# Kernel optimization log

Measured on AMD Instinct MI355X. Metric: run time of the kernel, lower is better.

The kernel has to match this reference:

```python
import jax, jax.numpy as jnp
import numpy as np

TOP_K = 5
EPS = 1e-12  # F.normalize eps

def _l2_normalize(v):
    n = jnp.linalg.norm(v, axis=-1, keepdims=True)
    return v / jnp.maximum(n, EPS)

def setup_inputs() -> dict:
    key = jax.random.key(0)
    k1, k2 = jax.random.split(key)
    B, S, C, M = 4, 2048, 512, 32768
    x = jax.random.normal(k1, (B, S, C), dtype=jnp.float32)
    # xavier_uniform-ish init for the memory table
    bound = np.sqrt(6.0 / (M + C)).astype(np.float32)
    memory_mean = jax.random.uniform(k2, (M, C), dtype=jnp.float32, minval=-bound, maxval=bound)
    return {"x": x, "memory_mean": memory_mean}

def reference(x, memory_mean):
    B, S, C = x.shape
    Mmat = memory_mean  # deterministic=True -> _sample_M returns memory_mean
    q = x.reshape(-1, C)                      # [BS, C]
    qn = _l2_normalize(q)
    mn = _l2_normalize(Mmat)                  # [M, C]
    sim = qn @ mn.T                           # [BS, M] cosine similarity
    scores, idx = jax.lax.top_k(sim, TOP_K)   # [BS, K]
    w = jax.nn.softmax(scores, axis=-1)       # [BS, K]
    gathered = Mmat[idx]                      # [BS, K, C]
    retrieved = jnp.einsum('bk,bkc->bc', w, gathered).reshape(B, S, C)
    out = x + 0.5 * retrieved
    return out
```

## Files before the change

kernel.cpp:

```cpp
#include <hip/hip_runtime.h>
#include <math.h>

using f32x4 = __attribute__((ext_vector_type(4))) float;
typedef __attribute__((ext_vector_type(4))) int i32x4;
typedef __attribute__((ext_vector_type(8))) int i32x8;
typedef unsigned char u8;

#define BS    8192
#define CDIM  512
#define MROWS 32768
#define NC    8
#define CHUNK (MROWS / NC)
#define TN    32
#define TQ    128
#define KTOP  5
#define ITERS (CHUNK / TN)
#define ROWB  512
#define KEY_INIT 0x3FFF8000u
#define SCL   0x7F7F7F7F

__device__ __forceinline__ unsigned enc_key(float s, int n) {
    unsigned u = __float_as_uint(s);
    u ^= (unsigned)((int)u >> 31) | 0x80000000u;
    return (u & 0xFFFF8000u) | (unsigned)n;
}
__device__ __forceinline__ float dec_score(unsigned k) {
    unsigned u = k & 0xFFFF8000u;
    u = (u & 0x80000000u) ? (u ^ 0x80000000u) : ~u;
    return __uint_as_float(u);
}

__device__ __forceinline__ void ins_nb(unsigned (&ks)[KTOP], unsigned k) {
    unsigned t = k;
#pragma unroll
    for (int j = 0; j < KTOP; ++j) {
        unsigned hi = t > ks[j] ? t : ks[j];
        unsigned lo = t > ks[j] ? ks[j] : t;
        ks[j] = hi; t = lo;
    }
}

__device__ __forceinline__ float dpp_fmax16(float x) {
    int t;
    t = __builtin_amdgcn_update_dpp(0, __float_as_int(x), 0xB1, 0xF, 0xF, true);
    x = fmaxf(x, __int_as_float(t));
    t = __builtin_amdgcn_update_dpp(0, __float_as_int(x), 0x4E, 0xF, 0xF, true);
    x = fmaxf(x, __int_as_float(t));
    t = __builtin_amdgcn_update_dpp(0, __float_as_int(x), 0x141, 0xF, 0xF, true);
    x = fmaxf(x, __int_as_float(t));
    t = __builtin_amdgcn_update_dpp(0, __float_as_int(x), 0x140, 0xF, 0xF, true);
    x = fmaxf(x, __int_as_float(t));
    return x;
}

__global__ void nrm_cast2(const float* __restrict__ memM, u8* __restrict__ mn,
                          const float* __restrict__ x, u8* __restrict__ qn) {
    int wave = threadIdx.x >> 6, lane = threadIdx.x & 63;
    int row = blockIdx.x * 4 + wave;
    const float* in;
    u8* out;
    if (row < MROWS) { in = memM + (size_t)row * CDIM; out = mn + (size_t)row * ROWB; }
    else             { int r = row - MROWS; in = x + (size_t)r * CDIM; out = qn + (size_t)r * ROWB; }
    const float* rp = in + lane * 8;
    float4 v0 = *(const float4*)rp;
    float4 v1 = *(const float4*)(rp + 4);
    float ss = v0.x * v0.x + v0.y * v0.y + v0.z * v0.z + v0.w * v0.w
             + v1.x * v1.x + v1.y * v1.y + v1.z * v1.z + v1.w * v1.w;
#pragma unroll
    for (int d = 1; d < 64; d <<= 1) ss += __shfl_xor(ss, d);
    float sc = 1.0f / fmaxf(sqrtf(ss), 1e-12f);
    int lo = __builtin_amdgcn_cvt_pk_fp8_f32(v0.x * sc, v0.y * sc, 0, false);
    lo     = __builtin_amdgcn_cvt_pk_fp8_f32(v0.z * sc, v0.w * sc, lo, true);
    int hi = __builtin_amdgcn_cvt_pk_fp8_f32(v1.x * sc, v1.y * sc, 0, false);
    hi     = __builtin_amdgcn_cvt_pk_fp8_f32(v1.z * sc, v1.w * sc, hi, true);
    uint2 o; o.x = (unsigned)lo; o.y = (unsigned)hi;
    *(uint2*)(out + lane * 8) = o;
}

__device__ __forceinline__ void stage_tile(const u8* __restrict__ mn, int nb,
                                           u8* buf, int wave, int lane) {
    const int r0 = wave * 8;
    const int li = lane & 31, half = lane >> 5;
#pragma unroll
    for (int j = 0; j < 4; ++j) {
        const int row = r0 + 2 * j + half;
        const u8* src = mn + (size_t)(nb + row) * ROWB + ((li ^ (row & 7)) * 16);
        __builtin_amdgcn_global_load_lds(
            (const __attribute__((address_space(1))) void*)src,
            (__attribute__((address_space(3))) void*)(buf + (r0 + 2 * j) * ROWB),
            16, 0, 0);
    }
}

__global__ __launch_bounds__(256, 2) void simtopk(
        const u8* __restrict__ qn, const u8* __restrict__ mn,
        unsigned* __restrict__ cand) {
    __shared__ __align__(16) u8 Bt[2][TN * ROWB];

    const int tid  = threadIdx.x;
    const int wave = tid >> 6, lane = tid & 63;
    const int quad = lane >> 4, c16 = lane & 15;
    const int nc = blockIdx.x;
    const int qt = blockIdx.y;
    const int qw = qt * TQ + wave * 32;
    const int nb0 = nc * CHUNK;

    i32x8 a[2][4];
#pragma unroll
    for (int s = 0; s < 2; ++s) {
        const u8* p = qn + (size_t)(qw + s * 16 + c16) * ROWB + quad * 32;
#pragma unroll
        for (int t = 0; t < 4; ++t) {
            i32x4 lo = *(const i32x4*)(p + t * 128);
            i32x4 hi = *(const i32x4*)(p + t * 128 + 16);
            a[s][t] = __builtin_shufflevector(lo, hi, 0, 1, 2, 3, 4, 5, 6, 7);
        }
    }

    unsigned keys[8][KTOP];
    float thr[8];
#pragma unroll
    for (int l = 0; l < 8; ++l) {
        thr[l] = -2.0f;
#pragma unroll
        for (int j = 0; j < KTOP; ++j) keys[l][j] = KEY_INIT;
    }

    const int sw  = c16 & 7;
    const int pb0 = c16 * ROWB + (((2 * quad) ^ sw) * 16);

    f32x4 p00 = {-2.f, -2.f, -2.f, -2.f};
    f32x4 p01 = p00, p10 = p00, p11 = p00;
    int np0 = nb0, np1 = nb0;

    stage_tile(mn, nb0, &Bt[0][0], wave, lane);

    for (int it = 0; it < ITERS; ++it) {
        __syncthreads();

        const u8* bb = &Bt[it & 1][0];
        f32x4 acc00 = {0.f, 0.f, 0.f, 0.f}, acc01 = {0.f, 0.f, 0.f, 0.f};
        f32x4 acc10 = {0.f, 0.f, 0.f, 0.f}, acc11 = {0.f, 0.f, 0.f, 0.f};
#pragma unroll
        for (int t = 0; t < 4; ++t) {
            i32x4 l0 = *(const i32x4*)(bb + pb0 + t * 128);
            i32x4 h0 = *(const i32x4*)(bb + (pb0 ^ 16) + t * 128);
            i32x8 b0 = __builtin_shufflevector(l0, h0, 0, 1, 2, 3, 4, 5, 6, 7);
            acc00 = __builtin_amdgcn_mfma_scale_f32_16x16x128_f8f6f4(
                        a[0][t], b0, acc00, 0, 0, 0, SCL, 0, SCL);
            acc10 = __builtin_amdgcn_mfma_scale_f32_16x16x128_f8f6f4(
                        a[1][t], b0, acc10, 0, 0, 0, SCL, 0, SCL);
            i32x4 l1 = *(const i32x4*)(bb + pb0 + 16 * ROWB + t * 128);
            i32x4 h1 = *(const i32x4*)(bb + (pb0 ^ 16) + 16 * ROWB + t * 128);
            i32x8 b1 = __builtin_shufflevector(l1, h1, 0, 1, 2, 3, 4, 5, 6, 7);
            acc01 = __builtin_amdgcn_mfma_scale_f32_16x16x128_f8f6f4(
                        a[0][t], b1, acc01, 0, 0, 0, SCL, 0, SCL);
            acc11 = __builtin_amdgcn_mfma_scale_f32_16x16x128_f8f6f4(
                        a[1][t], b1, acc11, 0, 0, 0, SCL, 0, SCL);
        }

        if (it + 1 < ITERS)
            stage_tile(mn, nb0 + (it + 1) * TN, &Bt[(it + 1) & 1][0], wave, lane);

#pragma unroll
        for (int j = 0; j < 4; ++j) {
            if (p00[j] > thr[j])     ins_nb(keys[j],     enc_key(p00[j], np0));
            if (p01[j] > thr[j])     ins_nb(keys[j],     enc_key(p01[j], np1));
            if (p10[j] > thr[4 + j]) ins_nb(keys[4 + j], enc_key(p10[j], np0));
            if (p11[j] > thr[4 + j]) ins_nb(keys[4 + j], enc_key(p11[j], np1));
        }
        if ((it & 3) == 3) {
#pragma unroll
            for (int l = 0; l < 8; ++l)
                thr[l] = dpp_fmax16(fmaxf(thr[l], dec_score(keys[l][KTOP - 1])));
        }

        p00 = acc00; p01 = acc01; p10 = acc10; p11 = acc11;
        np0 = nb0 + it * TN + c16;
        np1 = np0 + 16;
    }

#pragma unroll
    for (int j = 0; j < 4; ++j) {
        if (p00[j] > thr[j])     ins_nb(keys[j],     enc_key(p00[j], np0));
        if (p01[j] > thr[j])     ins_nb(keys[j],     enc_key(p01[j], np1));
        if (p10[j] > thr[4 + j]) ins_nb(keys[4 + j], enc_key(p10[j], np0));
        if (p11[j] > thr[4 + j]) ins_nb(keys[4 + j], enc_key(p11[j], np1));
    }

#pragma unroll
    for (int d = 1; d <= 8; d <<= 1) {
#pragma unroll
        for (int l = 0; l < 8; ++l) {
            unsigned rk[KTOP];
#pragma unroll
            for (int j = 0; j < KTOP; ++j) rk[j] = (unsigned)__shfl_xor((int)keys[l][j], d);
#pragma unroll
            for (int j = 0; j < KTOP; ++j) ins_nb(keys[l], rk[j]);
        }
    }

#pragma unroll
    for (int l = 0; l < 8; ++l) {
        if (c16 == l) {
            const int q = qw + (l >> 2) * 16 + quad * 4 + (l & 3);
            unsigned* cp = cand + ((size_t)q * NC + nc) * KTOP;
#pragma unroll
            for (int j = 0; j < KTOP; ++j) cp[j] = keys[l][j];
        }
    }
}

__global__ void epilogue(const float* __restrict__ x, const float* __restrict__ mem,
                         const unsigned* __restrict__ cand, float* __restrict__ out) {
    int wave = threadIdx.x >> 6, lane = threadIdx.x & 63;
    int q = blockIdx.x * 4 + wave;

    unsigned key = (lane < NC * KTOP) ? cand[(size_t)q * (NC * KTOP) + lane] : 0u;
    float s[KTOP]; int id[KTOP];
#pragma unroll
    for (int k = 0; k < KTOP; ++k) {
        unsigned m = key;
#pragma unroll
        for (int d = 32; d; d >>= 1) {
            unsigned o = (unsigned)__shfl_xor((int)m, d);
            m = o > m ? o : m;
        }
        s[k] = dec_score(m);
        id[k] = (int)(m & 0x7FFFu);
        unsigned long long b = __ballot(key == m);
        int first = __ffsll((long long)b) - 1;
        if (lane == first) key = 0u;
    }
    float w[KTOP], sum = 0.f;
#pragma unroll
    for (int k = 0; k < KTOP; ++k) { w[k] = expf(s[k] - s[0]); sum += w[k]; }
    float inv = 0.5f / sum;

    int c = lane * 8;
    const float4* xp = (const float4*)(x + (size_t)q * CDIM + c);
    float4 o0 = xp[0], o1 = xp[1];
#pragma unroll
    for (int k = 0; k < KTOP; ++k) {
        float wk = w[k] * inv;
        const float4* mp = (const float4*)(mem + (size_t)id[k] * CDIM + c);
        float4 g0 = mp[0], g1 = mp[1];
        o0.x += wk * g0.x; o0.y += wk * g0.y; o0.z += wk * g0.z; o0.w += wk * g0.w;
        o1.x += wk * g1.x; o1.y += wk * g1.y; o1.z += wk * g1.z; o1.w += wk * g1.w;
    }
    float* op = out + (size_t)q * CDIM + c;
    *(float4*)op = o0;
    *(float4*)(op + 4) = o1;
}

extern "C" void kernel_launch(void* const* d_in, const int* in_sizes, int n_in,
                              void* d_out, int out_size, void* d_ws, size_t ws_size,
                              hipStream_t stream) {
    const float* x    = (const float*)d_in[0];
    const float* memM = (const float*)d_in[1];
    float* out = (float*)d_out;

    u8* mn = (u8*)d_ws;
    u8* qn = mn + (size_t)MROWS * ROWB;
    unsigned* cand = (unsigned*)(qn + (size_t)BS * ROWB);

    nrm_cast2<<<(MROWS + BS) / 4, 256, 0, stream>>>(memM, mn, x, qn);
    simtopk<<<dim3(NC, BS / TQ), 256, 0, stream>>>(qn, mn, cand);
    epilogue<<<BS / 4, 256, 0, stream>>>(x, memM, cand, out);
}
```

Baseline: 339.9 us.

## Drop threshold-gated top-k insertion and raise priority around MFMA block

Removes the per-lane score thresholds and their periodic DPP max-reduction, so every candidate score is now inserted into the branchless top-5 network unconditionally. This avoids divergent branches and the threshold bookkeeping, but it adds roughly 5 compare-swap steps per candidate where most candidates used to be rejected. It also wraps the MFMA loop in s_setprio(1)/s_setprio(0) to favour matrix issue over other waves.

```diff
diff --git a/kernel.cpp b/kernel.cpp
--- a/kernel.cpp
+++ b/kernel.cpp
@@ -38,19 +38,6 @@
         unsigned lo = t > ks[j] ? ks[j] : t;
         ks[j] = hi; t = lo;
     }
-}
-
-__device__ __forceinline__ float dpp_fmax16(float x) {
-    int t;
-    t = __builtin_amdgcn_update_dpp(0, __float_as_int(x), 0xB1, 0xF, 0xF, true);
-    x = fmaxf(x, __int_as_float(t));
-    t = __builtin_amdgcn_update_dpp(0, __float_as_int(x), 0x4E, 0xF, 0xF, true);
-    x = fmaxf(x, __int_as_float(t));
-    t = __builtin_amdgcn_update_dpp(0, __float_as_int(x), 0x141, 0xF, 0xF, true);
-    x = fmaxf(x, __int_as_float(t));
-    t = __builtin_amdgcn_update_dpp(0, __float_as_int(x), 0x140, 0xF, 0xF, true);
-    x = fmaxf(x, __int_as_float(t));
-    return x;
 }
 
 __global__ void nrm_cast2(const float* __restrict__ memM, u8* __restrict__ mn,
@@ -118,13 +105,10 @@
     }
 
     unsigned keys[8][KTOP];
-    float thr[8];
-#pragma unroll
-    for (int l = 0; l < 8; ++l) {
-        thr[l] = -2.0f;
+#pragma unroll
+    for (int l = 0; l < 8; ++l)
 #pragma unroll
         for (int j = 0; j < KTOP; ++j) keys[l][j] = KEY_INIT;
-    }
 
     const int sw  = c16 & 7;
     const int pb0 = c16 * ROWB + (((2 * quad) ^ sw) * 16);
@@ -141,6 +125,7 @@
         const u8* bb = &Bt[it & 1][0];
         f32x4 acc00 = {0.f, 0.f, 0.f, 0.f}, acc01 = {0.f, 0.f, 0.f, 0.f};
         f32x4 acc10 = {0.f, 0.f, 0.f, 0.f}, acc11 = {0.f, 0.f, 0.f, 0.f};
+        __builtin_amdgcn_s_setprio(1);
 #pragma unroll
         for (int t = 0; t < 4; ++t) {
             i32x4 l0 = *(const i32x4*)(bb + pb0 + t * 128);
@@ -158,21 +143,17 @@
             acc11 = __builtin_amdgcn_mfma_scale_f32_16x16x128_f8f6f4(
                         a[1][t], b1, acc11, 0, 0, 0, SCL, 0, SCL);
         }
+        __builtin_amdgcn_s_setprio(0);
 
         if (it + 1 < ITERS)
             stage_tile(mn, nb0 + (it + 1) * TN, &Bt[(it + 1) & 1][0], wave, lane);
 
 #pragma unroll
         for (int j = 0; j < 4; ++j) {
-            if (p00[j] > thr[j])     ins_nb(keys[j],     enc_key(p00[j], np0));
-            if (p01[j] > thr[j])     ins_nb(keys[j],     enc_key(p01[j], np1));
-            if (p10[j] > thr[4 + j]) ins_nb(keys[4 + j], enc_key(p10[j], np0));
-            if (p11[j] > thr[4 + j]) ins_nb(keys[4 + j], enc_key(p11[j], np1));
-        }
-        if ((it & 3) == 3) {
-#pragma unroll
-            for (int l = 0; l < 8; ++l)
-                thr[l] = dpp_fmax16(fmaxf(thr[l], dec_score(keys[l][KTOP - 1])));
+            ins_nb(keys[j],     enc_key(p00[j], np0));
+            ins_nb(keys[j],     enc_key(p01[j], np1));
+            ins_nb(keys[4 + j], enc_key(p10[j], np0));
+            ins_nb(keys[4 + j], enc_key(p11[j], np1));
         }
 
         p00 = acc00; p01 = acc01; p10 = acc10; p11 = acc11;
@@ -182,10 +163,10 @@
 
 #pragma unroll
     for (int j = 0; j < 4; ++j) {
-        if (p00[j] > thr[j])     ins_nb(keys[j],     enc_key(p00[j], np0));
-        if (p01[j] > thr[j])     ins_nb(keys[j],     enc_key(p01[j], np1));
-        if (p10[j] > thr[4 + j]) ins_nb(keys[4 + j], enc_key(p10[j], np0));
-        if (p11[j] > thr[4 + j]) ins_nb(keys[4 + j], enc_key(p11[j], np1));
+        ins_nb(keys[j],     enc_key(p00[j], np0));
+        ins_nb(keys[j],     enc_key(p01[j], np1));
+        ins_nb(keys[4 + j], enc_key(p10[j], np0));
+        ins_nb(keys[4 + j], enc_key(p11[j], np1));
     }
 
 #pragma unroll
```

Measured after the change: 299.6 us, median of 2. -11.9%, faster.
